# Kernel tuning notes

Hardware: AMD Instinct MI355X
Metric: run time of the kernel (lower is better)

Reference implementation:

```python
import jax, jax.numpy as jnp
import numpy as np
import math

V = 32000; SMAX = 256; N = 512; M = 16; TICKS = 4; D = 512
NSA = 256; NSO = 512; H = 8; HD = D // H; B = 2; S = 256


def _ln(x, g, b, eps=1e-5):
    m = x.mean(-1, keepdims=True)
    v = ((x - m) ** 2).mean(-1, keepdims=True)
    return (x - m) / jnp.sqrt(v + eps) * g + b


def _glu(x):
    a, b = jnp.split(x, 2, axis=-1)
    return a * jax.nn.sigmoid(b)


def setup_inputs() -> dict:
    key = jax.random.key(0)
    ks = iter(jax.random.split(key, 64))
    rn = lambda shape, s: jax.random.normal(next(ks), shape, jnp.float32) * s
    inp = {}
    inp['x'] = jax.random.randint(next(ks), (B, S), 0, V)
    inp['tok_table'] = rn((V, D), 0.02)
    inp['pos_embed'] = rn((SMAX, D), 0.02)
    inp['ln_emb_g'] = jnp.ones(D); inp['ln_emb_b'] = jnp.zeros(D)
    inp['kv_w'] = rn((D, D), 1 / math.sqrt(D)); inp['kv_b'] = jnp.zeros(D)
    inp['kv_ln_g'] = jnp.ones(D); inp['kv_ln_b'] = jnp.zeros(D)
    inp['q_w'] = rn((NSA, D), 1 / math.sqrt(NSA)); inp['q_b'] = jnp.zeros(D)
    inp['wq'] = rn((D, D), 1 / math.sqrt(D)); inp['bq'] = jnp.zeros(D)
    inp['wk'] = rn((D, D), 1 / math.sqrt(D)); inp['bk'] = jnp.zeros(D)
    inp['wv'] = rn((D, D), 1 / math.sqrt(D)); inp['bv'] = jnp.zeros(D)
    inp['ow'] = rn((D, D), 1 / math.sqrt(D)); inp['ob'] = jnp.zeros(D)
    inp['syn_w'] = rn((D + N, 2 * N), 1 / math.sqrt(D + N)); inp['syn_b'] = jnp.zeros(2 * N)
    inp['syn_g'] = jnp.ones(N); inp['syn_beta'] = jnp.zeros(N)
    inp['fc1_w'] = rn((N, M, 256), math.sqrt(2.0 / M)); inp['fc1_b'] = jnp.zeros((N, 256))
    inp['fc2_w'] = rn((N, 128, 2), math.sqrt(2.0 / 128)); inp['fc2_b'] = jnp.zeros((N, 2))
    inp['nlm_T'] = jnp.ones(1)
    a = math.sqrt(1.0 / N)
    inp['start_act'] = jax.random.uniform(next(ks), (SMAX, N), jnp.float32, -a, a)
    b2 = math.sqrt(1.0 / (N + M))
    inp['start_trace'] = jax.random.uniform(next(ks), (SMAX, N, M), jnp.float32, -b2, b2)
    inp['decay_a'] = jnp.zeros(NSA); inp['decay_o'] = jnp.zeros(NSO)
    inp['out_w'] = rn((NSO, V), 1 / math.sqrt(NSO)); inp['out_b'] = jnp.zeros(V)
    inp['idx_al'] = jax.random.randint(next(ks), (NSA,), 0, N)
    inp['idx_ar'] = jax.random.randint(next(ks), (NSA,), 0, N)
    inp['idx_ol'] = jax.random.randint(next(ks), (NSO,), 0, N)
    inp['idx_or'] = jax.random.randint(next(ks), (NSO,), 0, N)
    return inp


def reference(x, tok_table, pos_embed, ln_emb_g, ln_emb_b, kv_w, kv_b, kv_ln_g, kv_ln_b,
              q_w, q_b, wq, bq, wk, bk, wv, bv, ow, ob, syn_w, syn_b, syn_g, syn_beta,
              fc1_w, fc1_b, fc2_w, fc2_b, nlm_T, start_act, start_trace, decay_a, decay_o,
              out_w, out_b, idx_al, idx_ar, idx_ol, idx_or):
    Bz, Sl = x.shape
    emb = _ln(tok_table[x] + pos_embed[:Sl], ln_emb_g, ln_emb_b)        # (B,S,D)
    kv = _ln(emb @ kv_w + kv_b, kv_ln_g, kv_ln_b)
    k = (kv @ wk + bk).reshape(Bz, Sl, H, HD)                            # keys/values fixed over ticks
    v = (kv @ wv + bv).reshape(Bz, Sl, H, HD)
    mask = jnp.triu(jnp.ones((Sl, Sl), bool), 1)                         # True = masked
    r_a = jnp.exp(-decay_a)
    r_o = jnp.exp(-decay_o)
    act = jnp.broadcast_to(start_act[:Sl], (Bz, Sl, N))
    trace = jnp.broadcast_to(start_trace[:Sl], (Bz, Sl, N, M))
    aa = ba = ao_ = bo = None
    preds, certs = [], []
    for _ in range(TICKS):
        # action synchronization (decayed pairwise product)
        pp = act[:, :, idx_al] * act[:, :, idx_ar]
        if aa is None:
            aa, ba = pp, jnp.ones_like(pp)
        else:
            aa, ba = r_a * aa + pp, r_a * ba + 1.0
        sync_a = aa / jnp.sqrt(ba + 1e-8)
        # causal attention with query from action sync
        qh = ((sync_a @ q_w + q_b) @ wq + bq).reshape(Bz, Sl, H, HD)
        sc = jnp.einsum('bqhd,bkhd->bhqk', qh, k) / math.sqrt(HD)
        sc = jnp.where(mask, -1e9, sc)
        attn_out = jnp.einsum('bhqk,bkhd->bqhd', jax.nn.softmax(sc, -1), v).reshape(Bz, Sl, D) @ ow + ob
        # synapse MLP -> new pre-activation, shift memory trace
        state = _ln(_glu(jnp.concatenate([attn_out, act], -1) @ syn_w + syn_b), syn_g, syn_beta)
        trace = jnp.concatenate([trace[..., 1:], state[..., None]], -1)
        # per-neuron NLM (batched private GEMMs)
        h = _glu(jnp.einsum('bsnm,nmh->bsnh', trace, fc1_w) + fc1_b)
        o = _glu(jnp.einsum('bsnh,nho->bsno', h, fc2_w) + fc2_b)
        act = o[..., 0] / nlm_T[0]
        # output synchronization + prediction
        ppo = act[:, :, idx_ol] * act[:, :, idx_or]
        if ao_ is None:
            ao_, bo = ppo, jnp.ones_like(ppo)
        else:
            ao_, bo = r_o * ao_ + ppo, r_o * bo + 1.0
        pred = (ao_ / jnp.sqrt(bo + 1e-8)) @ out_w + out_b                # (B,S,V)
        p = jax.nn.softmax(pred, -1)
        ent = -(p * jnp.log(p + 1e-10)).sum(-1) / math.log(V)
        preds.append(pred)
        certs.append(jnp.stack([ent, 1.0 - ent], -1))
    return jnp.stack(preds, -1), jnp.stack(certs, -1)
```

## Files before the change

### kernel.cpp

```cpp
#include <hip/hip_runtime.h>
#include <cstdint>
#include <cstddef>

#define BATCH 2
#define SEQ   256
#define DIM   512
#define NN    512
#define MM    16
#define NTICK 4
#define NSA   256
#define NSO   512
#define NHEAD 8
#define HDIM  64
#define VOCAB 32000
#define BS    (BATCH*SEQ)
#define NBLK  250

typedef __bf16 bf16;
typedef bf16  bf16x4  __attribute__((ext_vector_type(4)));
typedef bf16  bf16x8v __attribute__((ext_vector_type(8)));
typedef float f32x4   __attribute__((ext_vector_type(4)));

__global__ __launch_bounds__(128) void embed_kernel(const int* __restrict__ x,
    const float* __restrict__ tok, const float* __restrict__ pos, float* __restrict__ out){
  int row = blockIdx.x;
  int s = row & (SEQ-1);
  int token = x[row];
  const float4* tr = (const float4*)(tok + (size_t)token*DIM);
  const float4* pr = (const float4*)(pos + (size_t)s*DIM);
  float4* orow = (float4*)(out + (size_t)row*DIM);
  for (int i = threadIdx.x; i < DIM/4; i += blockDim.x){
    float4 a = tr[i], b = pr[i];
    float4 o; o.x=a.x+b.x; o.y=a.y+b.y; o.z=a.z+b.z; o.w=a.w+b.w;
    orow[i] = o;
  }
}

__global__ __launch_bounds__(256) void ln512_kernel(const float* __restrict__ in,
    const float* __restrict__ g, const float* __restrict__ b, float* __restrict__ out){
  int row = blockIdx.x, tid = threadIdx.x;
  const float* xr = in + (size_t)row*512;
  float v0 = xr[tid], v1 = xr[tid+256];
  float s = v0+v1, ss = v0*v0+v1*v1;
  #pragma unroll
  for (int o = 32; o > 0; o >>= 1){ s += __shfl_down(s, o); ss += __shfl_down(ss, o); }
  __shared__ float rs[4], rss[4];
  __shared__ float smean, sinv;
  int wid = tid >> 6, lane = tid & 63;
  if (lane == 0){ rs[wid] = s; rss[wid] = ss; }
  __syncthreads();
  if (tid == 0){
    float S = rs[0]+rs[1]+rs[2]+rs[3];
    float SS = rss[0]+rss[1]+rss[2]+rss[3];
    float m = S * (1.0f/512.0f);
    float var = SS * (1.0f/512.0f) - m*m;
    smean = m; sinv = 1.0f/sqrtf(var + 1e-5f);
  }
  __syncthreads();
  float m = smean, inv = sinv;
  out[(size_t)row*512 + tid]       = (v0-m)*inv*g[tid]     + b[tid];
  out[(size_t)row*512 + tid + 256] = (v1-m)*inv*g[tid+256] + b[tid+256];
}

__global__ __launch_bounds__(256) void glu_ln_kernel(const float* __restrict__ y,
    const float* __restrict__ g, const float* __restrict__ beta, float* __restrict__ out){
  int row = blockIdx.x, tid = threadIdx.x;
  const float* yr = y + (size_t)row*1024;
  float a0 = yr[tid],     b0 = yr[tid+512];
  float a1 = yr[tid+256], b1 = yr[tid+768];
  float g0 = a0 / (1.0f + expf(-b0));
  float g1 = a1 / (1.0f + expf(-b1));
  float s = g0+g1, ss = g0*g0+g1*g1;
  #pragma unroll
  for (int o = 32; o > 0; o >>= 1){ s += __shfl_down(s, o); ss += __shfl_down(ss, o); }
  __shared__ float rs[4], rss[4];
  __shared__ float smean, sinv;
  int wid = tid >> 6, lane = tid & 63;
  if (lane == 0){ rs[wid] = s; rss[wid] = ss; }
  __syncthreads();
  if (tid == 0){
    float S = rs[0]+rs[1]+rs[2]+rs[3];
    float SS = rss[0]+rss[1]+rss[2]+rss[3];
    float m = S * (1.0f/512.0f);
    float var = SS * (1.0f/512.0f) - m*m;
    smean = m; sinv = 1.0f/sqrtf(var + 1e-5f);
  }
  __syncthreads();
  float m = smean, inv = sinv;
  out[(size_t)row*512 + tid]       = (g0-m)*inv*g[tid]     + beta[tid];
  out[(size_t)row*512 + tid + 256] = (g1-m)*inv*g[tid+256] + beta[tid+256];
}

__global__ __launch_bounds__(256) void sync_kernel(const float* __restrict__ act,
    const int* __restrict__ il, const int* __restrict__ ir, const float* __restrict__ decay,
    float* __restrict__ accA, float* __restrict__ accB,
    float* __restrict__ outf, bf16* __restrict__ outb, int NS, int first){
  int i = blockIdx.x*256 + threadIdx.x;
  if (i >= BS*NS) return;
  int bs = i / NS, c = i - bs*NS;
  const float* ar = act + (size_t)bs*NN;
  float p = ar[il[c]] * ar[ir[c]];
  float A, Bv;
  if (first){ A = p; Bv = 1.0f; }
  else {
    float r = expf(-decay[c]);
    A = r*accA[i] + p;
    Bv = r*accB[i] + 1.0f;
  }
  accA[i] = A; accB[i] = Bv;
  float sy = A / sqrtf(Bv + 1e-8f);
  if (outf) outf[i] = sy;
  if (outb) outb[i] = (bf16)sy;
}

__global__ __launch_bounds__(256) void split_t(const float* __restrict__ W,
    bf16* __restrict__ hiT, bf16* __restrict__ loT, int K, int N){
  __shared__ float t[32][33];
  int n0 = blockIdx.x*32, k0 = blockIdx.y*32;
  int tid = threadIdx.x;
  int r = tid >> 3, c4 = (tid & 7)*4;
  float4 v = *(const float4*)(W + (size_t)(k0+r)*N + n0 + c4);
  t[r][c4+0]=v.x; t[r][c4+1]=v.y; t[r][c4+2]=v.z; t[r][c4+3]=v.w;
  __syncthreads();
  bf16x4 hi, lo;
  #pragma unroll
  for (int j = 0; j < 4; j++){
    float a = t[c4+j][r];
    bf16 h = (bf16)a;
    hi[j] = h;
    lo[j] = (bf16)(a - (float)h);
  }
  *(bf16x4*)(hiT + (size_t)(n0+r)*K + k0 + c4) = hi;
  if (loT) *(bf16x4*)(loT + (size_t)(n0+r)*K + k0 + c4) = lo;
}

__global__ __launch_bounds__(64) void gemm_x3(
    const float* __restrict__ A, const bf16* __restrict__ WhT,
    const bf16* __restrict__ WlT, const float* __restrict__ bias,
    float* __restrict__ C, int K, int lda, int ldc){
  int n0 = blockIdx.x * 64, m0 = blockIdx.y * 16;
  int lane = threadIdx.x;
  int ln = lane & 15, kq = lane >> 4;
  f32x4 acc[4];
  #pragma unroll
  for (int nf = 0; nf < 4; nf++) acc[nf] = (f32x4){0.f,0.f,0.f,0.f};
  const float* arow = A + (size_t)(m0 + ln)*lda + kq*8;
  const bf16* w0h = WhT + (size_t)(n0 + ln)*K + kq*8;
  const bf16* w0l = WlT + (size_t)(n0 + ln)*K + kq*8;
  size_t nstep = (size_t)16*K;
  for (int k0 = 0; k0 < K; k0 += 32){
    float4 a0 = *(const float4*)(arow + k0);
    float4 a1 = *(const float4*)(arow + k0 + 4);
    float av[8] = {a0.x,a0.y,a0.z,a0.w,a1.x,a1.y,a1.z,a1.w};
    bf16x8v ahi, alo;
    #pragma unroll
    for (int j = 0; j < 8; j++){
      bf16 h = (bf16)av[j];
      ahi[j] = h;
      alo[j] = (bf16)(av[j] - (float)h);
    }
    #pragma unroll
    for (int nf = 0; nf < 4; nf++){
      bf16x8v bh = *(const bf16x8v*)(w0h + nf*nstep + k0);
      bf16x8v bl = *(const bf16x8v*)(w0l + nf*nstep + k0);
      acc[nf] = __builtin_amdgcn_mfma_f32_16x16x32_bf16(ahi, bh, acc[nf], 0,0,0);
      acc[nf] = __builtin_amdgcn_mfma_f32_16x16x32_bf16(alo, bh, acc[nf], 0,0,0);
      acc[nf] = __builtin_amdgcn_mfma_f32_16x16x32_bf16(ahi, bl, acc[nf], 0,0,0);
    }
  }
  #pragma unroll
  for (int nf = 0; nf < 4; nf++){
    int col = n0 + nf*16 + ln;
    float bb = bias ? bias[col] : 0.0f;
    #pragma unroll
    for (int r = 0; r < 4; r++)
      C[(size_t)(m0 + kq*4 + r)*ldc + col] = acc[nf][r] + bb;
  }
}

__global__ void qbc_kernel(const float* __restrict__ qb, const float* __restrict__ wq,
                           const float* __restrict__ bq, float* __restrict__ qbc){
  int j = blockIdx.x*64 + threadIdx.x;
  float s = bq[j];
  for (int k = 0; k < DIM; k++) s = fmaf(qb[k], wq[(size_t)k*DIM + j], s);
  qbc[j] = s;
}

__global__ __launch_bounds__(256) void attn_kernel(const float* __restrict__ qh,
    const float* __restrict__ kb, const float* __restrict__ vb, float* __restrict__ outb){
  int qt = blockIdx.x, h = blockIdx.y, b = blockIdx.z;
  __shared__ float qs[16][HDIM];
  __shared__ float sc[16][SEQ + 4];
  __shared__ float red[16][16];
  __shared__ float rowm[16], rowz[16];
  int tid = threadIdx.x;
  {
    int r = tid >> 4, c4 = tid & 15;
    *(float4*)&qs[r][c4*4] =
      *(const float4*)(qh + ((size_t)(b*SEQ + qt*16 + r))*DIM + h*HDIM + c4*4);
  }
  __syncthreads();
  {
    int kk = tid;
    const float* krow = kb + ((size_t)(b*SEQ + kk))*DIM + h*HDIM;
    float s[16] = {};
    for (int d4 = 0; d4 < HDIM/4; d4++){
      float4 k4 = *(const float4*)(krow + d4*4);
      #pragma unroll
      for (int q = 0; q < 16; q++){
        float4 q4 = *(const float4*)&qs[q][d4*4];
        s[q] += q4.x*k4.x + q4.y*k4.y + q4.z*k4.z + q4.w*k4.w;
      }
    }
    #pragma unroll
    for (int q = 0; q < 16; q++){
      int qg = qt*16 + q;
      sc[q][kk] = (kk > qg) ? -1e9f : s[q]*0.125f;
    }
  }
  __syncthreads();
  {
    int q = tid >> 4, seg = tid & 15;
    float m = -1e30f;
    for (int i = 0; i < 16; i++) m = fmaxf(m, sc[q][seg*16+i]);
    red[q][seg] = m;
  }
  __syncthreads();
  if (tid < 16){
    float m = red[tid][0];
    for (int i = 1; i < 16; i++) m = fmaxf(m, red[tid][i]);
    rowm[tid] = m;
  }
  __syncthreads();
  {
    int q = tid >> 4, seg = tid & 15;
    float m = rowm[q], z = 0.0f;
    for (int i = 0; i < 16; i++){
      float e = expf(sc[q][seg*16+i] - m);
      sc[q][seg*16+i] = e;
      z += e;
    }
    red[q][seg] = z;
  }
  __syncthreads();
  if (tid < 16){
    float z = 0.0f;
    for (int i = 0; i < 16; i++) z += red[tid][i];
    rowz[tid] = 1.0f / z;
  }
  __syncthreads();
  {
    int q = tid >> 4, dc = tid & 15;
    float inv = rowz[q];
    float ax=0, ay=0, az=0, aw=0;
    for (int kk = 0; kk < SEQ; kk++){
      float p = sc[q][kk];
      float4 v4 = *(const float4*)(vb + ((size_t)(b*SEQ + kk))*DIM + h*HDIM + dc*4);
      ax = fmaf(p, v4.x, ax); ay = fmaf(p, v4.y, ay);
      az = fmaf(p, v4.z, az); aw = fmaf(p, v4.w, aw);
    }
    float4 o; o.x=ax*inv; o.y=ay*inv; o.z=az*inv; o.w=aw*inv;
    *(float4*)(outb + ((size_t)(b*SEQ + qt*16 + q))*DIM + h*HDIM + dc*4) = o;
  }
}

__global__ void act_init_kernel(const float* __restrict__ sa, float* __restrict__ act){
  int i = blockIdx.x*256 + threadIdx.x;
  act[i] = sa[i & (SEQ*NN - 1)];
}
__global__ void cat_act_kernel(const float* __restrict__ act, float* __restrict__ cat){
  int i = blockIdx.x*256 + threadIdx.x;
  int bs = i >> 9, n = i & 511;
  cat[(size_t)bs*1024 + 512 + n] = act[i];
}

__global__ __launch_bounds__(256) void nlm_kernel(
    const float* __restrict__ start_trace,
    const float* __restrict__ s0, const float* __restrict__ s1,
    const float* __restrict__ s2, const float* __restrict__ s3,
    const float* __restrict__ fc1w, const float* __restrict__ fc1b,
    const float* __restrict__ fc2w, const float* __restrict__ fc2b,
    const float* __restrict__ nlmT, float* __restrict__ act, int t){
  int n = blockIdx.x, b = blockIdx.y, s = threadIdx.x;
  int bs = b*SEQ + s;
  size_t sidx = (size_t)bs*NN + n;
  float tr[16];
  #pragma unroll
  for (int j = 0; j < 16; j++){
    int src = j + t + 1;
    if (src < 16){
      tr[j] = start_trace[((size_t)s*NN + n)*MM + src];
    } else {
      int k = src - 16;
      tr[j] = (k==0) ? s0[sidx] : (k==1) ? s1[sidx] : (k==2) ? s2[sidx] : s3[sidx];
    }
  }
  const float* w1 = fc1w + (size_t)n*16*256;
  const float* b1 = fc1b + (size_t)n*256;
  const float* w2 = fc2w + (size_t)n*256;
  float o0 = fc2b[n*2+0], o1 = fc2b[n*2+1];
  #pragma unroll 4
  for (int j = 0; j < 128; j++){
    float a  = b1[j];
    float bb = b1[j+128];
    #pragma unroll
    for (int m = 0; m < 16; m++){
      a  = fmaf(tr[m], w1[m*256 + j],       a);
      bb = fmaf(tr[m], w1[m*256 + j + 128], bb);
    }
    float gg = a / (1.0f + expf(-bb));
    o0 = fmaf(gg, w2[j*2+0], o0);
    o1 = fmaf(gg, w2[j*2+1], o1);
  }
  float o = o0 / (1.0f + expf(-o1));
  act[sidx] = o / nlmT[0];
}

__global__ __launch_bounds__(256) void out_gemm2(
    const bf16* __restrict__ sy0, const bf16* __restrict__ sy1,
    const bf16* __restrict__ sy2, const bf16* __restrict__ sy3,
    const bf16* __restrict__ WoT, const float* __restrict__ bo,
    float* __restrict__ outp, float* __restrict__ pm,
    float* __restrict__ pz, float* __restrict__ ps){
  int m0 = blockIdx.x * 16;
  int n0 = blockIdx.y * 128;
  int tid = threadIdx.x;
  int w = tid >> 6, lane = tid & 63;
  int ln = lane & 15, kq = lane >> 4;
  int nb = n0 + w*32;
  f32x4 acc[4][2];
  #pragma unroll
  for (int t = 0; t < 4; t++){
    acc[t][0] = (f32x4){0.f,0.f,0.f,0.f};
    acc[t][1] = (f32x4){0.f,0.f,0.f,0.f};
  }
  size_t aoff = (size_t)(m0 + ln)*512 + kq*8;
  const bf16* a0p = sy0 + aoff;
  const bf16* a1p = sy1 + aoff;
  const bf16* a2p = sy2 + aoff;
  const bf16* a3p = sy3 + aoff;
  const bf16* b0p = WoT + (size_t)(nb + ln)*512 + kq*8;
  const bf16* b1p = b0p + (size_t)16*512;
  for (int k0 = 0; k0 < 512; k0 += 32){
    bf16x8v av0 = *(const bf16x8v*)(a0p + k0);
    bf16x8v av1 = *(const bf16x8v*)(a1p + k0);
    bf16x8v av2 = *(const bf16x8v*)(a2p + k0);
    bf16x8v av3 = *(const bf16x8v*)(a3p + k0);
    bf16x8v bv0 = *(const bf16x8v*)(b0p + k0);
    bf16x8v bv1 = *(const bf16x8v*)(b1p + k0);
    acc[0][0] = __builtin_amdgcn_mfma_f32_16x16x32_bf16(av0, bv0, acc[0][0], 0,0,0);
    acc[1][0] = __builtin_amdgcn_mfma_f32_16x16x32_bf16(av1, bv0, acc[1][0], 0,0,0);
    acc[2][0] = __builtin_amdgcn_mfma_f32_16x16x32_bf16(av2, bv0, acc[2][0], 0,0,0);
    acc[3][0] = __builtin_amdgcn_mfma_f32_16x16x32_bf16(av3, bv0, acc[3][0], 0,0,0);
    acc[0][1] = __builtin_amdgcn_mfma_f32_16x16x32_bf16(av0, bv1, acc[0][1], 0,0,0);
    acc[1][1] = __builtin_amdgcn_mfma_f32_16x16x32_bf16(av1, bv1, acc[1][1], 0,0,0);
    acc[2][1] = __builtin_amdgcn_mfma_f32_16x16x32_bf16(av2, bv1, acc[2][1], 0,0,0);
    acc[3][1] = __builtin_amdgcn_mfma_f32_16x16x32_bf16(av3, bv1, acc[3][1], 0,0,0);
  }
  float bb0 = bo[nb + ln], bb1 = bo[nb + 16 + ln];
  #pragma unroll
  for (int t = 0; t < 4; t++)
    #pragma unroll
    for (int r = 0; r < 4; r++){ acc[t][0][r] += bb0; acc[t][1][r] += bb1; }
  #pragma unroll
  for (int r = 0; r < 4; r++){
    size_t rowoff = (size_t)(m0 + kq*4 + r)*VOCAB;
    float4 o0, o1;
    o0.x=acc[0][0][r]; o0.y=acc[1][0][r]; o0.z=acc[2][0][r]; o0.w=acc[3][0][r];
    o1.x=acc[0][1][r]; o1.y=acc[1][1][r]; o1.z=acc[2][1][r]; o1.w=acc[3][1][r];
    *(float4*)(outp + (rowoff + nb + ln)*4)      = o0;
    *(float4*)(outp + (rowoff + nb + 16 + ln)*4) = o1;
  }
  __shared__ float redm[4][4][16], redz[4][4][16], reds[4][4][16];
  float gm[4][4];
  #pragma unroll
  for (int t = 0; t < 4; t++)
    #pragma unroll
    for (int r = 0; r < 4; r++){
      float m = fmaxf(acc[t][0][r], acc[t][1][r]);
      #pragma unroll
      for (int o2 = 1; o2 < 16; o2 <<= 1) m = fmaxf(m, __shfl_xor(m, o2));
      gm[t][r] = m;
    }
  if (ln == 0){
    #pragma unroll
    for (int t = 0; t < 4; t++)
      #pragma unroll
      for (int r = 0; r < 4; r++) redm[w][t][kq*4+r] = gm[t][r];
  }
  __syncthreads();
  #pragma unroll
  for (int t = 0; t < 4; t++)
    #pragma unroll
    for (int r = 0; r < 4; r++){
      int row = kq*4+r;
      gm[t][r] = fmaxf(fmaxf(redm[0][t][row], redm[1][t][row]),
                       fmaxf(redm[2][t][row], redm[3][t][row]));
    }
  float zz[4][4], ssv[4][4];
  #pragma unroll
  for (int t = 0; t < 4; t++)
    #pragma unroll
    for (int r = 0; r < 4; r++){
      float v0 = acc[t][0][r] - gm[t][r];
      float v1 = acc[t][1][r] - gm[t][r];
      float e0 = expf(v0), e1 = expf(v1);
      float z = e0 + e1;
      float s = v0*e0 + v1*e1;
      #pragma unroll
      for (int o2 = 1; o2 < 16; o2 <<= 1){ z += __shfl_xor(z, o2); s += __shfl_xor(s, o2); }
      zz[t][r] = z; ssv[t][r] = s;
    }
  if (ln == 0){
    #pragma unroll
    for (int t = 0; t < 4; t++)
      #pragma unroll
      for (int r = 0; r < 4; r++){ redz[w][t][kq*4+r] = zz[t][r]; reds[w][t][kq*4+r] = ssv[t][r]; }
  }
  __syncthreads();
  if (w == 0 && ln == 0){
    #pragma unroll
    for (int t = 0; t < 4; t++)
      #pragma unroll
      for (int r = 0; r < 4; r++){
        int row = kq*4 + r;
        float Z = redz[0][t][row]+redz[1][t][row]+redz[2][t][row]+redz[3][t][row];
        float S = reds[0][t][row]+reds[1][t][row]+reds[2][t][row]+reds[3][t][row];
        size_t p = ((size_t)(m0+row)*4 + t)*NBLK + blockIdx.y;
        pm[p] = gm[t][r]; pz[p] = Z; ps[p] = S;
      }
  }
}

__global__ __launch_bounds__(64) void ent_final(const float* __restrict__ pm,
    const float* __restrict__ pz, const float* __restrict__ ps, float* __restrict__ certs){
  int row = blockIdx.x >> 2, t = blockIdx.x & 3;
  const size_t base = ((size_t)row*4 + t)*NBLK;
  int lane = threadIdx.x;
  float M = -1e30f, Z = 0.0f, S = 0.0f;
  for (int i = lane; i < NBLK; i += 64){
    float m2 = pm[base+i], z2 = pz[base+i], s2 = ps[base+i];
    float Mn = fmaxf(M, m2);
    float e1 = expf(M - Mn), e2 = expf(m2 - Mn);
    S = (S + (M - Mn)*Z)*e1 + (s2 + (m2 - Mn)*z2)*e2;
    Z = Z*e1 + z2*e2;
    M = Mn;
  }
  #pragma unroll
  for (int o = 1; o < 64; o <<= 1){
    float m2 = __shfl_xor(M, o), z2 = __shfl_xor(Z, o), s2 = __shfl_xor(S, o);
    float Mn = fmaxf(M, m2);
    float e1 = expf(M - Mn), e2 = expf(m2 - Mn);
    S = (S + (M - Mn)*Z)*e1 + (s2 + (m2 - Mn)*z2)*e2;
    Z = Z*e1 + z2*e2;
    M = Mn;
  }
  if (lane == 0){
    float ent = (logf(Z) - S/Z) * (1.0f / logf((float)VOCAB));
    certs[((size_t)row*2 + 0)*4 + t] = ent;
    certs[((size_t)row*2 + 1)*4 + t] = 1.0f - ent;
  }
}

extern "C" void kernel_launch(void* const* d_in, const int* in_sizes, int n_in,
                              void* d_out, int out_size, void* d_ws, size_t ws_size,
                              hipStream_t stream){
  const int*   x        = (const int*)  d_in[0];
  const float* tok      = (const float*)d_in[1];
  const float* pos      = (const float*)d_in[2];
  const float* ln_emb_g = (const float*)d_in[3];
  const float* ln_emb_b = (const float*)d_in[4];
  const float* kv_w     = (const float*)d_in[5];
  const float* kv_b     = (const float*)d_in[6];
  const float* kv_ln_g  = (const float*)d_in[7];
  const float* kv_ln_b  = (const float*)d_in[8];
  const float* q_w      = (const float*)d_in[9];
  const float* q_b      = (const float*)d_in[10];
  const float* wq       = (const float*)d_in[11];
  const float* bq       = (const float*)d_in[12];
  const float* wk       = (const float*)d_in[13];
  const float* bk       = (const float*)d_in[14];
  const float* wv       = (const float*)d_in[15];
  const float* bv       = (const float*)d_in[16];
  const float* ow       = (const float*)d_in[17];
  const float* ob       = (const float*)d_in[18];
  const float* syn_w    = (const float*)d_in[19];
  const float* syn_b    = (const float*)d_in[20];
  const float* syn_g    = (const float*)d_in[21];
  const float* syn_beta = (const float*)d_in[22];
  const float* fc1_w    = (const float*)d_in[23];
  const float* fc1_b    = (const float*)d_in[24];
  const float* fc2_w    = (const float*)d_in[25];
  const float* fc2_b    = (const float*)d_in[26];
  const float* nlm_T    = (const float*)d_in[27];
  const float* start_act   = (const float*)d_in[28];
  const float* start_trace = (const float*)d_in[29];
  const float* decay_a  = (const float*)d_in[30];
  const float* decay_o  = (const float*)d_in[31];
  const float* out_w    = (const float*)d_in[32];
  const float* out_b    = (const float*)d_in[33];
  const int* idx_al = (const int*)d_in[34];
  const int* idx_ar = (const int*)d_in[35];
  const int* idx_ol = (const int*)d_in[36];
  const int* idx_or = (const int*)d_in[37];

  char* wp = (char*)d_ws;
  auto alloc = [&](size_t bytes) -> void* {
    void* p = (void*)wp;
    wp += (bytes + 255) & ~(size_t)255;
    return p;
  };
  float* qwc      = (float*)alloc((size_t)256*512*4);
  float* qbc      = (float*)alloc(512*4);
  float* emb_raw  = (float*)alloc((size_t)BS*512*4);
  float* emb      = (float*)alloc((size_t)BS*512*4);
  float* kvt      = (float*)alloc((size_t)BS*512*4);
  float* kvn      = (float*)alloc((size_t)BS*512*4);
  float* kbuf     = (float*)alloc((size_t)BS*512*4);
  float* vbuf     = (float*)alloc((size_t)BS*512*4);
  float* act      = (float*)alloc((size_t)BS*512*4);
  float* aaB      = (float*)alloc((size_t)BS*256*4);
  float* baB      = (float*)alloc((size_t)BS*256*4);
  float* aoB      = (float*)alloc((size_t)BS*512*4);
  float* boB      = (float*)alloc((size_t)BS*512*4);
  float* sync_a   = (float*)alloc((size_t)BS*256*4);
  float* qh       = (float*)alloc((size_t)BS*512*4);
  float* attn_raw = (float*)alloc((size_t)BS*512*4);
  float* catb     = (float*)alloc((size_t)BS*1024*4);
  float* syn_y    = (float*)alloc((size_t)BS*1024*4);
  float* states[NTICK];
  for (int t = 0; t < NTICK; t++) states[t] = (float*)alloc((size_t)BS*512*4);
  bf16* syob[NTICK];
  for (int t = 0; t < NTICK; t++) syob[t] = (bf16*)alloc((size_t)BS*512*2);
  bf16* kvT_h = (bf16*)alloc((size_t)512*512*2);
  bf16* kvT_l = (bf16*)alloc((size_t)512*512*2);
  bf16* wkT_h = (bf16*)alloc((size_t)512*512*2);
  bf16* wkT_l = (bf16*)alloc((size_t)512*512*2);
  bf16* wvT_h = (bf16*)alloc((size_t)512*512*2);
  bf16* wvT_l = (bf16*)alloc((size_t)512*512*2);
  bf16* owT_h = (bf16*)alloc((size_t)512*512*2);
  bf16* owT_l = (bf16*)alloc((size_t)512*512*2);
  bf16* wqT_h = (bf16*)alloc((size_t)512*512*2);
  bf16* wqT_l = (bf16*)alloc((size_t)512*512*2);
  bf16* synT_h = (bf16*)alloc((size_t)1024*1024*2);
  bf16* synT_l = (bf16*)alloc((size_t)1024*1024*2);
  bf16* qwcT_h = (bf16*)alloc((size_t)512*256*2);
  bf16* qwcT_l = (bf16*)alloc((size_t)512*256*2);
  bf16* WoT    = (bf16*)alloc((size_t)VOCAB*512*2);
  float* pm = (float*)alloc((size_t)BS*4*NBLK*4);
  float* pz = (float*)alloc((size_t)BS*4*NBLK*4);
  float* ps = (float*)alloc((size_t)BS*4*NBLK*4);

  float* preds = (float*)d_out;
  float* certs = (float*)d_out + (size_t)BS*VOCAB*NTICK;

  split_t<<<dim3(16,16), 256, 0, stream>>>(kv_w,  kvT_h, kvT_l, 512, 512);
  split_t<<<dim3(16,16), 256, 0, stream>>>(wk,    wkT_h, wkT_l, 512, 512);
  split_t<<<dim3(16,16), 256, 0, stream>>>(wv,    wvT_h, wvT_l, 512, 512);
  split_t<<<dim3(16,16), 256, 0, stream>>>(ow,    owT_h, owT_l, 512, 512);
  split_t<<<dim3(16,16), 256, 0, stream>>>(wq,    wqT_h, wqT_l, 512, 512);
  split_t<<<dim3(32,32), 256, 0, stream>>>(syn_w, synT_h, synT_l, 1024, 1024);
  split_t<<<dim3(VOCAB/32,16), 256, 0, stream>>>(out_w, WoT, nullptr, 512, VOCAB);

  embed_kernel<<<BS, 128, 0, stream>>>(x, tok, pos, emb_raw);
  ln512_kernel<<<BS, 256, 0, stream>>>(emb_raw, ln_emb_g, ln_emb_b, emb);
  gemm_x3<<<dim3(8,32), 64, 0, stream>>>(emb, kvT_h, kvT_l, kv_b, kvt, 512, 512, 512);
  ln512_kernel<<<BS, 256, 0, stream>>>(kvt, kv_ln_g, kv_ln_b, kvn);
  gemm_x3<<<dim3(8,32), 64, 0, stream>>>(kvn, wkT_h, wkT_l, bk, kbuf, 512, 512, 512);
  gemm_x3<<<dim3(8,32), 64, 0, stream>>>(kvn, wvT_h, wvT_l, bv, vbuf, 512, 512, 512);
  gemm_x3<<<dim3(8,16), 64, 0, stream>>>(q_w, wqT_h, wqT_l, nullptr, qwc, 512, 512, 512);
  split_t<<<dim3(16,8), 256, 0, stream>>>(qwc, qwcT_h, qwcT_l, 256, 512);
  qbc_kernel<<<8, 64, 0, stream>>>(q_b, wq, bq, qbc);
  act_init_kernel<<<(BS*NN)/256, 256, 0, stream>>>(start_act, act);

  for (int t = 0; t < NTICK; t++){
    sync_kernel<<<(BS*NSA)/256, 256, 0, stream>>>(act, idx_al, idx_ar, decay_a,
        aaB, baB, sync_a, nullptr, NSA, t==0);
    gemm_x3<<<dim3(8,32), 64, 0, stream>>>(sync_a, qwcT_h, qwcT_l, qbc, qh, 256, 256, 512);
    attn_kernel<<<dim3(16, NHEAD, BATCH), 256, 0, stream>>>(qh, kbuf, vbuf, attn_raw);
    gemm_x3<<<dim3(8,32), 64, 0, stream>>>(attn_raw, owT_h, owT_l, ob, catb, 512, 512, 1024);
    cat_act_kernel<<<(BS*NN)/256, 256, 0, stream>>>(act, catb);
    gemm_x3<<<dim3(16,32), 64, 0, stream>>>(catb, synT_h, synT_l, syn_b, syn_y, 1024, 1024, 1024);
    glu_ln_kernel<<<BS, 256, 0, stream>>>(syn_y, syn_g, syn_beta, states[t]);
    nlm_kernel<<<dim3(NN, BATCH), 256, 0, stream>>>(start_trace,
        states[0], states[1], states[2], states[3],
        fc1_w, fc1_b, fc2_w, fc2_b, nlm_T, act, t);
    sync_kernel<<<(BS*NSO)/256, 256, 0, stream>>>(act, idx_ol, idx_or, decay_o,
        aoB, boB, nullptr, syob[t], NSO, t==0);
  }

  out_gemm2<<<dim3(32, NBLK), 256, 0, stream>>>(
      syob[0], syob[1], syob[2], syob[3], WoT, out_b, preds, pm, pz, ps);
  ent_final<<<BS*4, 64, 0, stream>>>(pm, pz, ps, certs);
}
```

Measured before the change: 1.568 ms.

## Stage 64-column weight slab in LDS and loop all rows per block

```diff
diff --git a/kernel.cpp b/kernel.cpp
--- a/kernel.cpp
+++ b/kernel.cpp
@@ -14,12 +14,15 @@
 #define HDIM  64
 #define VOCAB 32000
 #define BS    (BATCH*SEQ)
-#define NBLK  250
+#define NBLK  500
 
 typedef __bf16 bf16;
 typedef bf16  bf16x4  __attribute__((ext_vector_type(4)));
 typedef bf16  bf16x8v __attribute__((ext_vector_type(8)));
 typedef float f32x4   __attribute__((ext_vector_type(4)));
+
+typedef __attribute__((address_space(1))) const void av1_t;
+typedef __attribute__((address_space(3))) void av3_t;
 
 __global__ __launch_bounds__(128) void embed_kernel(const int* __restrict__ x,
     const float* __restrict__ tok, const float* __restrict__ pos, float* __restrict__ out){
@@ -316,119 +319,124 @@
   act[sidx] = o / nlmT[0];
 }
 
-__global__ __launch_bounds__(256) void out_gemm2(
+__global__ __launch_bounds__(256) void out_gemm3(
     const bf16* __restrict__ sy0, const bf16* __restrict__ sy1,
     const bf16* __restrict__ sy2, const bf16* __restrict__ sy3,
     const bf16* __restrict__ WoT, const float* __restrict__ bo,
     float* __restrict__ outp, float* __restrict__ pm,
     float* __restrict__ pz, float* __restrict__ ps){
-  int m0 = blockIdx.x * 16;
-  int n0 = blockIdx.y * 128;
+  __shared__ bf16 Bs[64*512];
   int tid = threadIdx.x;
   int w = tid >> 6, lane = tid & 63;
   int ln = lane & 15, kq = lane >> 4;
-  int nb = n0 + w*32;
-  f32x4 acc[4][2];
-  #pragma unroll
-  for (int t = 0; t < 4; t++){
-    acc[t][0] = (f32x4){0.f,0.f,0.f,0.f};
-    acc[t][1] = (f32x4){0.f,0.f,0.f,0.f};
-  }
-  size_t aoff = (size_t)(m0 + ln)*512 + kq*8;
-  const bf16* a0p = sy0 + aoff;
-  const bf16* a1p = sy1 + aoff;
-  const bf16* a2p = sy2 + aoff;
-  const bf16* a3p = sy3 + aoff;
-  const bf16* b0p = WoT + (size_t)(nb + ln)*512 + kq*8;
-  const bf16* b1p = b0p + (size_t)16*512;
-  for (int k0 = 0; k0 < 512; k0 += 32){
-    bf16x8v av0 = *(const bf16x8v*)(a0p + k0);
-    bf16x8v av1 = *(const bf16x8v*)(a1p + k0);
-    bf16x8v av2 = *(const bf16x8v*)(a2p + k0);
-    bf16x8v av3 = *(const bf16x8v*)(a3p + k0);
-    bf16x8v bv0 = *(const bf16x8v*)(b0p + k0);
-    bf16x8v bv1 = *(const bf16x8v*)(b1p + k0);
-    acc[0][0] = __builtin_amdgcn_mfma_f32_16x16x32_bf16(av0, bv0, acc[0][0], 0,0,0);
-    acc[1][0] = __builtin_amdgcn_mfma_f32_16x16x32_bf16(av1, bv0, acc[1][0], 0,0,0);
-    acc[2][0] = __builtin_amdgcn_mfma_f32_16x16x32_bf16(av2, bv0, acc[2][0], 0,0,0);
-    acc[3][0] = __builtin_amdgcn_mfma_f32_16x16x32_bf16(av3, bv0, acc[3][0], 0,0,0);
-    acc[0][1] = __builtin_amdgcn_mfma_f32_16x16x32_bf16(av0, bv1, acc[0][1], 0,0,0);
-    acc[1][1] = __builtin_amdgcn_mfma_f32_16x16x32_bf16(av1, bv1, acc[1][1], 0,0,0);
-    acc[2][1] = __builtin_amdgcn_mfma_f32_16x16x32_bf16(av2, bv1, acc[2][1], 0,0,0);
-    acc[3][1] = __builtin_amdgcn_mfma_f32_16x16x32_bf16(av3, bv1, acc[3][1], 0,0,0);
-  }
-  float bb0 = bo[nb + ln], bb1 = bo[nb + 16 + ln];
-  #pragma unroll
-  for (int t = 0; t < 4; t++)
-    #pragma unroll
-    for (int r = 0; r < 4; r++){ acc[t][0][r] += bb0; acc[t][1][r] += bb1; }
-  #pragma unroll
-  for (int r = 0; r < 4; r++){
-    size_t rowoff = (size_t)(m0 + kq*4 + r)*VOCAB;
-    float4 o0, o1;
-    o0.x=acc[0][0][r]; o0.y=acc[1][0][r]; o0.z=acc[2][0][r]; o0.w=acc[3][0][r];
-    o1.x=acc[0][1][r]; o1.y=acc[1][1][r]; o1.z=acc[2][1][r]; o1.w=acc[3][1][r];
-    *(float4*)(outp + (rowoff + nb + ln)*4)      = o0;
-    *(float4*)(outp + (rowoff + nb + 16 + ln)*4) = o1;
-  }
-  __shared__ float redm[4][4][16], redz[4][4][16], reds[4][4][16];
-  float gm[4][4];
-  #pragma unroll
-  for (int t = 0; t < 4; t++)
-    #pragma unroll
-    for (int r = 0; r < 4; r++){
-      float m = fmaxf(acc[t][0][r], acc[t][1][r]);
+  int n0 = blockIdx.x * 64;
+
+  {
+    const char* gp = (const char*)(WoT + (size_t)n0*512);
+    char* lp = (char*)Bs;
+    #pragma unroll
+    for (int it = 0; it < 16; ++it){
+      int ub = (w*16 + it) << 10;
+      int b  = ub + lane*16;
+      int src = b ^ (((b >> 10) & 7) << 4);
+      __builtin_amdgcn_global_load_lds((av1_t*)(gp + src), (av3_t*)(lp + ub),
+                                       16, 0, 0);
+    }
+  }
+  __syncthreads();
+
+  float bb[4];
+  #pragma unroll
+  for (int nf = 0; nf < 4; ++nf) bb[nf] = bo[n0 + nf*16 + ln];
+
+  const size_t aoff = (size_t)ln*512 + (size_t)kq*8;
+  const char* Bsc = (const char*)Bs;
+  const int bbase = (ln << 10) + (kq << 4);
+  const int sw = (ln & 7) << 4;
+
+  for (int i = 0; i < 8; ++i){
+    int m0 = w*16 + i*64;
+    const bf16* pa0 = sy0 + (size_t)m0*512 + aoff;
+    const bf16* pa1 = sy1 + (size_t)m0*512 + aoff;
+    const bf16* pa2 = sy2 + (size_t)m0*512 + aoff;
+    const bf16* pa3 = sy3 + (size_t)m0*512 + aoff;
+    f32x4 acc[4][4];
+    #pragma unroll
+    for (int t = 0; t < 4; ++t)
       #pragma unroll
-      for (int o2 = 1; o2 < 16; o2 <<= 1) m = fmaxf(m, __shfl_xor(m, o2));
-      gm[t][r] = m;
-    }
-  if (ln == 0){
-    #pragma unroll
-    for (int t = 0; t < 4; t++)
+      for (int nf = 0; nf < 4; ++nf) acc[t][nf] = (f32x4){0.f,0.f,0.f,0.f};
+
+    #pragma unroll
+    for (int k0 = 0; k0 < 512; k0 += 32){
+      bf16x8v a0 = *(const bf16x8v*)(pa0 + k0);
+      bf16x8v a1 = *(const bf16x8v*)(pa1 + k0);
+      bf16x8v a2 = *(const bf16x8v*)(pa2 + k0);
+      bf16x8v a3 = *(const bf16x8v*)(pa3 + k0);
+      int kb = bbase + k0*2;
+      bf16x8v b0 = *(const bf16x8v*)(Bsc + ((kb           ) ^ sw));
+      bf16x8v b1 = *(const bf16x8v*)(Bsc + ((kb + 16*1024) ^ sw));
+      bf16x8v b2 = *(const bf16x8v*)(Bsc + ((kb + 32*1024) ^ sw));
+      bf16x8v b3 = *(const bf16x8v*)(Bsc + ((kb + 48*1024) ^ sw));
+      acc[0][0] = __builtin_amdgcn_mfma_f32_16x16x32_bf16(a0, b0, acc[0][0], 0,0,0);
+      acc[1][0] = __builtin_amdgcn_mfma_f32_16x16x32_bf16(a1, b0, acc[1][0], 0,0,0);
+      acc[2][0] = __builtin_amdgcn_mfma_f32_16x16x32_bf16(a2, b0, acc[2][0], 0,0,0);
+      acc[3][0] = __builtin_amdgcn_mfma_f32_16x16x32_bf16(a3, b0, acc[3][0], 0,0,0);
+      acc[0][1] = __builtin_amdgcn_mfma_f32_16x16x32_bf16(a0, b1, acc[0][1], 0,0,0);
+      acc[1][1] = __builtin_amdgcn_mfma_f32_16x16x32_bf16(a1, b1, acc[1][1], 0,0,0);
+      acc[2][1] = __builtin_amdgcn_mfma_f32_16x16x32_bf16(a2, b1, acc[2][1], 0,0,0);
+      acc[3][1] = __builtin_amdgcn_mfma_f32_16x16x32_bf16(a3, b1, acc[3][1], 0,0,0);
+      acc[0][2] = __builtin_amdgcn_mfma_f32_16x16x32_bf16(a0, b2, acc[0][2], 0,0,0);
+      acc[1][2] = __builtin_amdgcn_mfma_f32_16x16x32_bf16(a1, b2, acc[1][2], 0,0,0);
+      acc[2][2] = __builtin_amdgcn_mfma_f32_16x16x32_bf16(a2, b2, acc[2][2], 0,0,0);
+      acc[3][2] = __builtin_amdgcn_mfma_f32_16x16x32_bf16(a3, b2, acc[3][2], 0,0,0);
+      acc[0][3] = __builtin_amdgcn_mfma_f32_16x16x32_bf16(a0, b3, acc[0][3], 0,0,0);
+      acc[1][3] = __builtin_amdgcn_mfma_f32_16x16x32_bf16(a1, b3, acc[1][3], 0,0,0);
+      acc[2][3] = __builtin_amdgcn_mfma_f32_16x16x32_bf16(a2, b3, acc[2][3], 0,0,0);
+      acc[3][3] = __builtin_amdgcn_mfma_f32_16x16x32_bf16(a3, b3, acc[3][3], 0,0,0);
+    }
+
+    #pragma unroll
+    for (int t = 0; t < 4; ++t)
       #pragma unroll
-      for (int r = 0; r < 4; r++) redm[w][t][kq*4+r] = gm[t][r];
-  }
-  __syncthreads();
-  #pragma unroll
-  for (int t = 0; t < 4; t++)
-    #pragma unroll
-    for (int r = 0; r < 4; r++){
-      int row = kq*4+r;
-      gm[t][r] = fmaxf(fmaxf(redm[0][t][row], redm[1][t][row]),
-                       fmaxf(redm[2][t][row], redm[3][t][row]));
-    }
-  float zz[4][4], ssv[4][4];
-  #pragma unroll
-  for (int t = 0; t < 4; t++)
-    #pragma unroll
-    for (int r = 0; r < 4; r++){
-      float v0 = acc[t][0][r] - gm[t][r];
-      float v1 = acc[t][1][r] - gm[t][r];
-      float e0 = expf(v0), e1 = expf(v1);
-      float z = e0 + e1;
-      float s = v0*e0 + v1*e1;
+      for (int nf = 0; nf < 4; ++nf)
+        #pragma unroll
+        for (int r = 0; r < 4; ++r) acc[t][nf][r] += bb[nf];
+
+    #pragma unroll
+    for (int r = 0; r < 4; ++r){
+      size_t rowoff = (size_t)(m0 + kq*4 + r)*VOCAB;
       #pragma unroll
-      for (int o2 = 1; o2 < 16; o2 <<= 1){ z += __shfl_xor(z, o2); s += __shfl_xor(s, o2); }
-      zz[t][r] = z; ssv[t][r] = s;
-    }
-  if (ln == 0){
-    #pragma unroll
-    for (int t = 0; t < 4; t++)
+      for (int nf = 0; nf < 4; ++nf){
+        float4 o;
+        o.x = acc[0][nf][r]; o.y = acc[1][nf][r];
+        o.z = acc[2][nf][r]; o.w = acc[3][nf][r];
+        *(float4*)(outp + (rowoff + n0 + nf*16 + ln)*4) = o;
+      }
+    }
+
+    #pragma unroll
+    for (int t = 0; t < 4; ++t){
       #pragma unroll
-      for (int r = 0; r < 4; r++){ redz[w][t][kq*4+r] = zz[t][r]; reds[w][t][kq*4+r] = ssv[t][r]; }
-  }
-  __syncthreads();
-  if (w == 0 && ln == 0){
-    #pragma unroll
-    for (int t = 0; t < 4; t++)
-      #pragma unroll
-      for (int r = 0; r < 4; r++){
-        int row = kq*4 + r;
-        float Z = redz[0][t][row]+redz[1][t][row]+redz[2][t][row]+redz[3][t][row];
-        float S = reds[0][t][row]+reds[1][t][row]+reds[2][t][row]+reds[3][t][row];
-        size_t p = ((size_t)(m0+row)*4 + t)*NBLK + blockIdx.y;
-        pm[p] = gm[t][r]; pz[p] = Z; ps[p] = S;
+      for (int r = 0; r < 4; ++r){
+        float m = fmaxf(fmaxf(acc[t][0][r], acc[t][1][r]),
+                        fmaxf(acc[t][2][r], acc[t][3][r]));
+        #pragma unroll
+        for (int o2 = 1; o2 < 16; o2 <<= 1) m = fmaxf(m, __shfl_xor(m, o2));
+        float z = 0.0f, s = 0.0f;
+        #pragma unroll
+        for (int nf = 0; nf < 4; ++nf){
+          float v = acc[t][nf][r] - m;
+          float e = expf(v);
+          z += e; s += v*e;
+        }
+        #pragma unroll
+        for (int o2 = 1; o2 < 16; o2 <<= 1){ z += __shfl_xor(z, o2); s += __shfl_xor(s, o2); }
+        if (ln == 0){
+          size_t p = ((size_t)(m0 + kq*4 + r)*4 + t)*NBLK + blockIdx.x;
+          pm[p] = m; pz[p] = z; ps[p] = s;
+        }
       }
+    }
   }
 }
 
@@ -589,7 +597,7 @@
         aoB, boB, nullptr, syob[t], NSO, t==0);
   }
 
-  out_gemm2<<<dim3(32, NBLK), 256, 0, stream>>>(
+  out_gemm3<<<dim3(NBLK), 256, 0, stream>>>(
       syob[0], syob[1], syob[2], syob[3], WoT, out_b, preds, pm, pz, ps);
   ent_final<<<BS*4, 64, 0, stream>>>(pm, pz, ps, certs);
 }
```

Result: faster. 1.449 ms (-7.6%).
